# Kernel optimization log

Hardware: AMD Instinct MI355X
Metric: run time of the kernel (lower is better)

The kernel has to match this reference:

```python
import jax, jax.numpy as jnp
import numpy as np

EMBED_DIM = 1024
N_HEADS = 16
HEAD_DIM = EMBED_DIM // N_HEADS
MAX_REL_POS = 2  # hardcoded in the torch module


def _rel_index(length_q, length_k):
    # final_mat[i, j] = clip(i - j, -p, p) + p  with i over k-range, j over q-range
    rq = jnp.arange(length_q)[None, :]
    rk = jnp.arange(length_k)[:, None]
    dist = jnp.clip(rk - rq, -MAX_REL_POS, MAX_REL_POS) + MAX_REL_POS
    return dist  # (len_k, len_q) int; square when len_q == len_k


def setup_inputs() -> dict:
    key = jax.random.key(0)
    ks = jax.random.split(key, 16)
    B, S, E, H, D = 4, 1024, EMBED_DIM, N_HEADS, HEAD_DIM
    xavier = lambda k, shape: jax.random.uniform(
        k, shape, jnp.float32, -1.0, 1.0) * np.sqrt(6.0 / (shape[0] + shape[1]))
    return {
        "query": jax.random.normal(ks[0], (B, S, E), jnp.float32),
        "key": jax.random.normal(ks[1], (B, S, E), jnp.float32),
        "value": jax.random.normal(ks[2], (B, S, E), jnp.float32),
        "Wq": xavier(ks[3], (E, E)), "bq": jnp.zeros((E,), jnp.float32),
        "Wk": xavier(ks[4], (E, E)), "bk": jnp.zeros((E,), jnp.float32),
        "Wv": xavier(ks[5], (E, E)), "bv": jnp.zeros((E,), jnp.float32),
        "Wo": xavier(ks[6], (E, E)), "bo": jnp.zeros((E,), jnp.float32),
        "rpk_table": xavier(ks[7], (2 * MAX_REL_POS + 1, D)),
        "rpv_table": xavier(ks[8], (2 * MAX_REL_POS + 1, D)),
    }


def reference(query, key, value, Wq, bq, Wk, bk, Wv, bv, Wo, bo, rpk_table, rpv_table):
    B, S, E = query.shape
    H, D = N_HEADS, HEAD_DIM
    q = query @ Wq.T + bq
    _k = key @ Wk.T + bk      # computed but unused (faithful to source bug)
    v = value @ Wv.T + bv

    qh = q.reshape(B, S, H, D).transpose(0, 2, 1, 3)   # b h s d
    vh = v.reshape(B, S, H, D).transpose(0, 2, 1, 3)

    # NOTE: source uses query for both sides of the dot product
    dots = jnp.einsum('bhqd,bhkd->bhqk', qh, qh)

    idx = _rel_index(S, S)                              # (S, S)
    rpk = rpk_table[idx]                                # (S, S, D)
    rp_dots = jnp.einsum('bhqd,qkd->bhqk', qh, rpk)

    scale = jnp.sqrt(jnp.asarray(D, q.dtype))
    attn = jax.nn.softmax((dots + rp_dots) / scale, axis=-1)

    weight1 = jnp.einsum('bhqk,bhkd->bhqd', attn, vh)
    rpv = rpv_table[idx]                                # (S, S, D)
    weight2 = jnp.einsum('bhqk,qkd->bhqd', attn, rpv)

    out = (weight1 + weight2).transpose(0, 2, 1, 3).reshape(B, S, E)
    return out @ Wo.T + bo
```

## Files before the change

kernel.cpp:

```cpp
#include <hip/hip_runtime.h>


typedef _Float16 v8h __attribute__((ext_vector_type(8)));
typedef _Float16 v4h __attribute__((ext_vector_type(4)));
typedef float    v4f __attribute__((ext_vector_type(4)));

#define MFMA_F16(A_, B_, C_) __builtin_amdgcn_mfma_f32_16x16x32_f16(A_, B_, C_, 0, 0, 0)

__device__ __forceinline__ void async_copy16(const void* g, void* l) {
    __builtin_amdgcn_global_load_lds(
        (const __attribute__((address_space(1))) void*)g,
        (__attribute__((address_space(3))) void*)l, 16, 0, 0);
}

__device__ __forceinline__ float exp2_hw(float x) {
#if __has_builtin(__builtin_amdgcn_exp2f)
    return __builtin_amdgcn_exp2f(x);
#else
    float r;
    asm("v_exp_f32 %0, %1" : "=v"(r) : "v"(x));
    return r;
#endif
}

__global__ __launch_bounds__(256) void cvt5_kernel(
    const float* __restrict__ s0, const float* __restrict__ s1,
    const float* __restrict__ s2, const float* __restrict__ s3,
    const float* __restrict__ s4,
    _Float16* __restrict__ d0, _Float16* __restrict__ d1,
    _Float16* __restrict__ d2, _Float16* __restrict__ d3,
    _Float16* __restrict__ d4,
    int n0, int n1, int n2, int n3, int n4)
{
    const float* s; _Float16* d; int n;
    switch (blockIdx.y) {
        case 0:  s = s0; d = d0; n = n0; break;
        case 1:  s = s1; d = d1; n = n1; break;
        case 2:  s = s2; d = d2; n = n2; break;
        case 3:  s = s3; d = d3; n = n3; break;
        default: s = s4; d = d4; n = n4; break;
    }
    int i = (blockIdx.x * 256 + threadIdx.x) * 4;
    if (i >= n) return;
    float4 f = *(const float4*)(s + i);
    v4h o = { (_Float16)f.x, (_Float16)f.y, (_Float16)f.z, (_Float16)f.w };
    *(v4h*)(d + i) = o;
}

template<int TM, int MODE>
__device__ __forceinline__ void gemm_core(const _Float16* __restrict__ A,
                                          const _Float16* __restrict__ W,
                                          const float* __restrict__ bias,
                                          void* __restrict__ outp,
                                          int row0, int col0)
{
    constexpr int WCOLS = (TM == 128) ? 64 : 32;
    constexpr int NJ = WCOLS / 16;
    constexpr int SC_H = (MODE == 2) ? 4096 : 64 * WCOLS;
    constexpr int STG_H = (TM + 128) * 64;
    constexpr int TOT_H = (STG_H > 4 * SC_H) ? STG_H : 4 * SC_H;
    __shared__ __align__(16) _Float16 smem[TOT_H];
    _Float16* As = smem;
    _Float16* Bs = smem + TM * 64;

    const int tid  = threadIdx.x;
    const int wave = tid >> 6, lane = tid & 63;
    const int quad = lane >> 4, n16 = lane & 15;
    const int wm = (TM == 128) ? (wave >> 1) : 0;
    const int wn = (TM == 128) ? (wave & 1) : wave;
    const int rL = lane >> 3, c8 = lane & 7;
    const int lcs = c8 ^ rL;

    v4f acc[4][NJ] = {};

    for (int kb = 0; kb < 1024; kb += 64) {
        __syncthreads();
        #pragma unroll
        for (int p = 0; p < TM / 32; p++) {
            int rg = wave * (TM / 32) + p;
            int row = rg * 8 + rL;
            async_copy16(A + (size_t)(row0 + row) * 1024 + kb + lcs * 8, &As[rg * 512]);
        }
        #pragma unroll
        for (int p = 0; p < 4; p++) {
            int rg = wave * 4 + p;
            int row = rg * 8 + rL;
            async_copy16(W + (size_t)(col0 + row) * 1024 + kb + lcs * 8, &Bs[rg * 512]);
        }
        __syncthreads();
        #pragma unroll
        for (int ks = 0; ks < 64; ks += 32) {
            const int pc = ((ks >> 3) + quad) ^ (n16 & 7);
            v8h af[4], bf[NJ];
            #pragma unroll
            for (int i = 0; i < 4; i++)
                af[i] = *(const v8h*)(&As[(wm * 64 + i * 16 + n16) * 64 + pc * 8]);
            #pragma unroll
            for (int j = 0; j < NJ; j++)
                bf[j] = *(const v8h*)(&Bs[(wn * WCOLS + j * 16 + n16) * 64 + pc * 8]);
            #pragma unroll
            for (int i = 0; i < 4; i++)
                #pragma unroll
                for (int j = 0; j < NJ; j++)
                    acc[i][j] = MFMA_F16(af[i], bf[j], acc[i][j]);
        }
    }

    __syncthreads();
    const int b     = (row0 + wm * 64) >> 10;
    const int srow0 = (row0 + wm * 64) & 1023;
    const int C0    = col0 + wn * WCOLS;

    if (MODE == 0) {
        _Float16* sc = smem + wave * SC_H;
        #pragma unroll
        for (int i = 0; i < 4; i++)
            #pragma unroll
            for (int j = 0; j < NJ; j++)
                #pragma unroll
                for (int r = 0; r < 4; r++) {
                    int rowL = i * 16 + quad * 4 + r, colL = j * 16 + n16;
                    float v = acc[i][j][r] + bias[C0 + colL];
                    sc[rowL * 64 + (((colL >> 3) ^ (rowL & 7)) << 3) + (colL & 7)] = (_Float16)v;
                }
        int h = C0 >> 6;
        #pragma unroll
        for (int it = 0; it < 8; it++) {
            int rowR = it * 8 + (lane >> 3), cR = lane & 7;
            v8h val = *(const v8h*)(&sc[rowR * 64 + ((cR ^ (rowR & 7)) << 3)]);
            *(v8h*)((_Float16*)outp +
                    (((size_t)(b * 16 + h) * 1024 + srow0 + rowR) << 6) + cR * 8) = val;
        }
    } else if (MODE == 1) {
        _Float16* sc = smem + wave * SC_H;
        #pragma unroll
        for (int i = 0; i < 4; i++)
            #pragma unroll
            for (int j = 0; j < NJ; j++) {
                int colL = j * 16 + n16;
                int c16 = i * 2 + (quad >> 1);
                v4h pk;
                #pragma unroll
                for (int r = 0; r < 4; r++)
                    pk[r] = (_Float16)(acc[i][j][r] + bias[C0 + colL]);
                *(v4h*)(&sc[colL * 64 + ((c16 ^ (colL & 7)) << 3) + (quad & 1) * 4]) = pk;
            }
        #pragma unroll
        for (int it = 0; it < 8; it++) {
            int dR = it * 8 + (lane >> 3), g = lane & 7;
            v8h val = *(const v8h*)(&sc[dR * 64 + ((g ^ (dR & 7)) << 3)]);
            int cg = C0 + dR;
            int h = cg >> 6, dl = cg & 63;
            _Float16* base = (_Float16*)outp +
                             ((size_t)((b * 16 + h) * 64 + dl) << 10) + srow0;
            int a4  = ((g >> 1) & 1) * 4, b32 = (g >> 2) * 32;
            int p0  = b32 + ((2 * g) & 3) * 8 + a4;
            int p1  = b32 + ((2 * g + 1) & 3) * 8 + a4;
            v4h lo = __builtin_shufflevector(val, val, 0, 1, 2, 3);
            v4h hi = __builtin_shufflevector(val, val, 4, 5, 6, 7);
            *(v4h*)(base + p0) = lo;
            *(v4h*)(base + p1) = hi;
        }
    } else {
        float* sc = (float*)smem + wave * 2048;
        #pragma unroll
        for (int i = 0; i < 4; i++)
            #pragma unroll
            for (int j = 0; j < 2; j++)
                #pragma unroll
                for (int r = 0; r < 4; r++) {
                    int rowL = i * 16 + quad * 4 + r, colL = j * 16 + n16;
                    sc[rowL * 32 + (((colL >> 2) ^ (rowL & 7)) << 2) + (colL & 3)] =
                        acc[i][j][r] + bias[col0 + wn * 32 + colL];
                }
        #pragma unroll
        for (int it = 0; it < 8; it++) {
            int rowR = it * 8 + (lane >> 3), cR = lane & 7;
            v4f val = *(const v4f*)(&sc[rowR * 32 + ((cR ^ (rowR & 7)) << 2)]);
            *(v4f*)((float*)outp + (size_t)(row0 + rowR) * 1024 + col0 + wn * 32 + cR * 4) = val;
        }
    }
}

__global__ __launch_bounds__(256) void gemm_qv_kernel(
    const _Float16* __restrict__ Aq, const _Float16* __restrict__ Av,
    const _Float16* __restrict__ Wq, const _Float16* __restrict__ Wv,
    const float* __restrict__ bq, const float* __restrict__ bv,
    _Float16* __restrict__ q_out, _Float16* __restrict__ v_out)
{
    int id = blockIdx.x;
    int y = (id & 7) | (((id >> 3) & 3) << 3);
    int x = (id >> 5) & 7;
    int z = id >> 8;
    if (z) gemm_core<128, 1>(Av, Wv, bv, (void*)v_out, y * 128, x * 128);
    else   gemm_core<128, 0>(Aq, Wq, bq, (void*)q_out, y * 128, x * 128);
}

__global__ __launch_bounds__(256) void gemm_o_kernel(
    const _Float16* __restrict__ A, const _Float16* __restrict__ W,
    const float* __restrict__ bias, float* __restrict__ outp)
{
    int id = blockIdx.x;
    int y = (id & 7) * 8 + ((id >> 3) & 7);
    int x = id >> 6;
    gemm_core<64, 2>(A, W, bias, (void*)outp, y * 64, x * 128);
}

__global__ __launch_bounds__(256, 4) void attn_kernel(
    const _Float16* __restrict__ qb,
    const _Float16* __restrict__ vt,
    const float* __restrict__ rpk, const float* __restrict__ rpv,
    _Float16* __restrict__ attn_o)
{
    const int blk = blockIdx.x;
    const int bh = blk & 63;
    const int q0 = (blk >> 6) * 64;
    const int tid = threadIdx.x;
    const int wave = tid >> 6, lane = tid & 63;
    const int quad = lane >> 4, n16 = lane & 15;
    const int qw = q0 + wave * 16;
    const _Float16* Qh = qb + (size_t)bh * 1024 * 64;
    const _Float16* Vh = vt + (size_t)bh * 64 * 1024;

    __shared__ __align__(16) _Float16 Ks[2][64 * 64];
    __shared__ __align__(16) _Float16 Vs[2][64 * 64];
    __shared__ float rqs[4][16][5];

    const int rL = lane >> 3, c8 = lane & 7;
    const int lcs = c8 ^ rL;

    #pragma unroll
    for (int p = 0; p < 2; p++) {
        int c = wave * 2 + p;
        int row = c * 8 + rL;
        async_copy16(Qh + (size_t)row * 64 + lcs * 8, &Ks[0][c * 512]);
        async_copy16(Vh + (size_t)row * 1024 + lcs * 8, &Vs[0][c * 512]);
    }

    {
        int m = lane >> 2, seg = lane & 3;
        const _Float16* qrow = Qh + (size_t)(qw + m) * 64 + seg * 16;
        v8h qa = *(const v8h*)(qrow);
        v8h qc = *(const v8h*)(qrow + 8);
        float qd[16];
        #pragma unroll
        for (int x = 0; x < 8; x++) { qd[x] = (float)qa[x]; qd[8 + x] = (float)qc[x]; }
        float qq = 0.f;
        #pragma unroll
        for (int x = 0; x < 16; x++) qq += qd[x] * qd[x];
        qq += __shfl_xor(qq, 1);
        qq += __shfl_xor(qq, 2);
        #pragma unroll
        for (int t = 0; t < 5; t++) {
            float s = 0.f;
            #pragma unroll
            for (int x = 0; x < 16; x++) s += qd[x] * rpk[t * 64 + seg * 16 + x];
            s += __shfl_xor(s, 1);
            s += __shfl_xor(s, 2);
            if (seg == 0) rqs[wave][m][t] = (s - qq) * 0.18033688736f;
        }
    }

    v8h aq0 = *(const v8h*)(Qh + (size_t)(qw + n16) * 64 + quad * 8);
    v8h aq1 = *(const v8h*)(Qh + (size_t)(qw + n16) * 64 + 32 + quad * 8);

    __syncthreads();

    float rc[5];
    #pragma unroll
    for (int t = 0; t < 5; t++) rc[t] = rqs[wave][n16][t];

    float bkt[5] = {0.f, 0.f, 0.f, 0.f, 0.f};
    v4f O[4] = {};

    const int pphys0 = quad ^ (n16 & 7);
    const int pphys1 = (quad + 4) ^ (n16 & 7);
    const float SCL = 0.18033688736f;

    for (int it = 0; it < 16; ++it) {
        const int cur = it & 1;
        const int kb = it * 64;
        if (it + 1 < 16) {
            const int nxt = 1 - cur;
            const int kn = kb + 64;
            #pragma unroll
            for (int p = 0; p < 2; p++) {
                int c = wave * 2 + p;
                int row = c * 8 + rL;
                async_copy16(Qh + (size_t)(kn + row) * 64 + lcs * 8, &Ks[nxt][c * 512]);
                async_copy16(Vh + (size_t)row * 1024 + kn + lcs * 8, &Vs[nxt][c * 512]);
            }
        }

        v8h ak0[4], ak1[4], av0[4], av1[4];
        #pragma unroll
        for (int t = 0; t < 4; t++) {
            ak0[t] = *(const v8h*)(&Ks[cur][(t * 16 + n16) * 64 + pphys0 * 8]);
            ak1[t] = *(const v8h*)(&Ks[cur][(t * 16 + n16) * 64 + pphys1 * 8]);
        }
        #pragma unroll
        for (int dt = 0; dt < 4; dt++) {
            av0[dt] = *(const v8h*)(&Vs[cur][(dt * 16 + n16) * 64 + pphys0 * 8]);
            av1[dt] = *(const v8h*)(&Vs[cur][(dt * 16 + n16) * 64 + pphys1 * 8]);
        }

        int pkLo[4], pkHi[4];
        #pragma unroll
        for (int t = 0; t < 4; t++) {
            v4f s = {0.f, 0.f, 0.f, 0.f};
            s = MFMA_F16(ak0[t], aq0, s);
            s = MFMA_F16(ak1[t], aq1, s);
            const int dqt = qw - kb - t * 16;
            float pv[4];
            if (dqt >= 17) {
                float p0 = exp2_hw(fmaf(s[0], SCL, rc[4]));
                float p1 = exp2_hw(fmaf(s[1], SCL, rc[4]));
                float p2 = exp2_hw(fmaf(s[2], SCL, rc[4]));
                float p3 = exp2_hw(fmaf(s[3], SCL, rc[4]));
                pv[0] = p0; pv[1] = p1; pv[2] = p2; pv[3] = p3;
                bkt[4] += (p0 + p1) + (p2 + p3);
            } else if (dqt <= -17) {
                float p0 = exp2_hw(fmaf(s[0], SCL, rc[0]));
                float p1 = exp2_hw(fmaf(s[1], SCL, rc[0]));
                float p2 = exp2_hw(fmaf(s[2], SCL, rc[0]));
                float p3 = exp2_hw(fmaf(s[3], SCL, rc[0]));
                pv[0] = p0; pv[1] = p1; pv[2] = p2; pv[3] = p3;
                bkt[0] += (p0 + p1) + (p2 + p3);
            } else {
                const int D0 = dqt + n16 - quad * 4;
                #pragma unroll
                for (int r = 0; r < 4; r++) {
                    int diff = D0 - r;
                    float rv = diff >= 2  ? rc[4]
                             : diff == 1  ? rc[3]
                             : diff == 0  ? rc[2]
                             : diff == -1 ? rc[1]
                                          : rc[0];
                    float p = exp2_hw(fmaf(s[r], SCL, rv));
                    pv[r] = p;
                    bkt[4] += (diff >= 2)  ? p : 0.f;
                    bkt[3] += (diff == 1)  ? p : 0.f;
                    bkt[2] += (diff == 0)  ? p : 0.f;
                    bkt[1] += (diff == -1) ? p : 0.f;
                    bkt[0] += (diff <= -2) ? p : 0.f;
                }
            }
            pkLo[t] = __builtin_bit_cast(int, __builtin_amdgcn_cvt_pkrtz(pv[0], pv[1]));
            pkHi[t] = __builtin_bit_cast(int, __builtin_amdgcn_cvt_pkrtz(pv[2], pv[3]));
        }

        union { int d[4]; v8h v; } ub0, ub1;
        ub0.d[0] = pkLo[0]; ub0.d[1] = pkHi[0]; ub0.d[2] = pkLo[1]; ub0.d[3] = pkHi[1];
        ub1.d[0] = pkLo[2]; ub1.d[1] = pkHi[2]; ub1.d[2] = pkLo[3]; ub1.d[3] = pkHi[3];
        v8h bf0 = ub0.v, bf1 = ub1.v;

        #pragma unroll
        for (int dt = 0; dt < 4; dt++) {
            O[dt] = MFMA_F16(av0[dt], bf0, O[dt]);
            O[dt] = MFMA_F16(av1[dt], bf1, O[dt]);
        }

        __syncthreads();
    }

    #pragma unroll
    for (int t = 0; t < 5; t++) {
        bkt[t] += __shfl_xor(bkt[t], 16);
        bkt[t] += __shfl_xor(bkt[t], 32);
    }
    float l = bkt[0] + bkt[1] + bkt[2] + bkt[3] + bkt[4];
    float inv = 1.0f / l;
    int q = qw + n16;
    size_t orow = (size_t)((bh >> 4) * 1024 + q) * 1024 + (bh & 15) * 64;
    #pragma unroll
    for (int dt = 0; dt < 4; dt++) {
        int d0 = dt * 16 + quad * 4;
        v4h st;
        #pragma unroll
        for (int r = 0; r < 4; r++) {
            int d = d0 + r;
            float w2 = bkt[4] * rpv[4 * 64 + d] + bkt[3] * rpv[3 * 64 + d]
                     + bkt[2] * rpv[2 * 64 + d] + bkt[1] * rpv[1 * 64 + d]
                     + bkt[0] * rpv[0 * 64 + d];
            st[r] = (_Float16)((O[dt][r] + w2) * inv);
        }
        *(v4h*)(attn_o + orow + d0) = st;
    }
}

extern "C" void kernel_launch(void* const* d_in, const int* in_sizes, int n_in,
                              void* d_out, int out_size, void* d_ws, size_t ws_size,
                              hipStream_t stream)
{
    const float* query = (const float*)d_in[0];
    const float* value = (const float*)d_in[2];
    const float* Wq = (const float*)d_in[3];
    const float* bq = (const float*)d_in[4];
    const float* Wv = (const float*)d_in[7];
    const float* bv = (const float*)d_in[8];
    const float* Wo = (const float*)d_in[9];
    const float* bo = (const float*)d_in[10];
    const float* rpk = (const float*)d_in[11];
    const float* rpv = (const float*)d_in[12];
    float* out = (float*)d_out;

    char* ws = (char*)d_ws;
    const size_t MB = 1024 * 1024;
    _Float16* q_bhsd = (_Float16*)(ws);
    _Float16* v_t    = (_Float16*)(ws + 8 * MB);
    _Float16* q16    = (_Float16*)(ws + 16 * MB);
    _Float16* attn_o = (_Float16*)(ws + 16 * MB);
    _Float16* v16    = (_Float16*)(ws + 24 * MB);
    _Float16* wq16   = (_Float16*)(ws + 32 * MB);
    _Float16* wv16   = (_Float16*)(ws + 34 * MB);
    _Float16* wo16   = (_Float16*)(ws + 36 * MB);

    cvt5_kernel<<<dim3(4096, 5), 256, 0, stream>>>(
        query, value, Wq, Wv, Wo, q16, v16, wq16, wv16, wo16,
        4096 * 1024, 4096 * 1024, 1024 * 1024, 1024 * 1024, 1024 * 1024);

    gemm_qv_kernel<<<dim3(512), 256, 0, stream>>>(
        q16, v16, wq16, wv16, bq, bv, q_bhsd, v_t);

    attn_kernel<<<dim3(1024), 256, 0, stream>>>(q_bhsd, v_t, rpk, rpv, attn_o);

    gemm_o_kernel<<<dim3(512), 256, 0, stream>>>(attn_o, wo16, bo, out);
}
```

Baseline: 196.0 us.

## Software-pipeline QK scores one tile ahead and single-buffer V in LDS

Restructures the attention loop so the QK^T MFMA scores for the next key tile are computed while the current tile's exponentials and PV products are processed. K tiles are prefetched two iterations ahead, and V is reduced to a single LDS buffer loaded at the start of each iteration. A second barrier is added mid-iteration before V is read. The aim is to overlap MFMA latency with the softmax VALU work and cut LDS use. In exchange, V loads are no longer prefetched across iterations, there are more barriers, and register pressure rises from holding two score sets.

```diff
diff --git a/kernel.cpp b/kernel.cpp
--- a/kernel.cpp
+++ b/kernel.cpp
@@ -223,7 +223,7 @@
     const _Float16* Vh = vt + (size_t)bh * 64 * 1024;
 
     __shared__ __align__(16) _Float16 Ks[2][64 * 64];
-    __shared__ __align__(16) _Float16 Vs[2][64 * 64];
+    __shared__ __align__(16) _Float16 Vs[64 * 64];
     __shared__ float rqs[4][16][5];
 
     const int rL = lane >> 3, c8 = lane & 7;
@@ -234,7 +234,7 @@
         int c = wave * 2 + p;
         int row = c * 8 + rL;
         async_copy16(Qh + (size_t)row * 64 + lcs * 8, &Ks[0][c * 512]);
-        async_copy16(Vh + (size_t)row * 1024 + lcs * 8, &Vs[0][c * 512]);
+        async_copy16(Qh + (size_t)(64 + row) * 64 + lcs * 8, &Ks[1][c * 512]);
     }
 
     {
@@ -270,46 +270,59 @@
     #pragma unroll
     for (int t = 0; t < 5; t++) rc[t] = rqs[wave][n16][t];
 
-    float bkt[5] = {0.f, 0.f, 0.f, 0.f, 0.f};
-    v4f O[4] = {};
-
     const int pphys0 = quad ^ (n16 & 7);
     const int pphys1 = (quad + 4) ^ (n16 & 7);
     const float SCL = 0.18033688736f;
 
+    v4f scur[4];
+    #pragma unroll
+    for (int t = 0; t < 4; t++) {
+        v8h k0 = *(const v8h*)(&Ks[0][(t * 16 + n16) * 64 + pphys0 * 8]);
+        v8h k1 = *(const v8h*)(&Ks[0][(t * 16 + n16) * 64 + pphys1 * 8]);
+        v4f s = {0.f, 0.f, 0.f, 0.f};
+        s = MFMA_F16(k0, aq0, s);
+        scur[t] = MFMA_F16(k1, aq1, s);
+    }
+    __syncthreads();
+
+    float bkt[5] = {0.f, 0.f, 0.f, 0.f, 0.f};
+    v4f O[4] = {};
+
     for (int it = 0; it < 16; ++it) {
-        const int cur = it & 1;
         const int kb = it * 64;
-        if (it + 1 < 16) {
-            const int nxt = 1 - cur;
-            const int kn = kb + 64;
+
+        #pragma unroll
+        for (int p = 0; p < 2; p++) {
+            int c = wave * 2 + p;
+            int row = c * 8 + rL;
+            async_copy16(Vh + (size_t)row * 1024 + kb + lcs * 8, &Vs[c * 512]);
+        }
+        if (it + 2 < 16) {
+            const int kn = kb + 128;
             #pragma unroll
             for (int p = 0; p < 2; p++) {
                 int c = wave * 2 + p;
                 int row = c * 8 + rL;
-                async_copy16(Qh + (size_t)(kn + row) * 64 + lcs * 8, &Ks[nxt][c * 512]);
-                async_copy16(Vh + (size_t)row * 1024 + kn + lcs * 8, &Vs[nxt][c * 512]);
+                async_copy16(Qh + (size_t)(kn + row) * 64 + lcs * 8, &Ks[it & 1][c * 512]);
             }
         }
 
-        v8h ak0[4], ak1[4], av0[4], av1[4];
+        v4f snx[4] = {};
+        if (it + 1 < 16) {
+            #pragma unroll
+            for (int t = 0; t < 4; t++) {
+                v8h k0 = *(const v8h*)(&Ks[(it + 1) & 1][(t * 16 + n16) * 64 + pphys0 * 8]);
+                v8h k1 = *(const v8h*)(&Ks[(it + 1) & 1][(t * 16 + n16) * 64 + pphys1 * 8]);
+                v4f s = {0.f, 0.f, 0.f, 0.f};
+                s = MFMA_F16(k0, aq0, s);
+                snx[t] = MFMA_F16(k1, aq1, s);
+            }
+        }
+
+        int pkLo[4], pkHi[4];
         #pragma unroll
         for (int t = 0; t < 4; t++) {
-            ak0[t] = *(const v8h*)(&Ks[cur][(t * 16 + n16) * 64 + pphys0 * 8]);
-            ak1[t] = *(const v8h*)(&Ks[cur][(t * 16 + n16) * 64 + pphys1 * 8]);
-        }
-        #pragma unroll
-        for (int dt = 0; dt < 4; dt++) {
-            av0[dt] = *(const v8h*)(&Vs[cur][(dt * 16 + n16) * 64 + pphys0 * 8]);
-            av1[dt] = *(const v8h*)(&Vs[cur][(dt * 16 + n16) * 64 + pphys1 * 8]);
-        }
-
-        int pkLo[4], pkHi[4];
-        #pragma unroll
-        for (int t = 0; t < 4; t++) {
-            v4f s = {0.f, 0.f, 0.f, 0.f};
-            s = MFMA_F16(ak0[t], aq0, s);
-            s = MFMA_F16(ak1[t], aq1, s);
+            const v4f s = scur[t];
             const int dqt = qw - kb - t * 16;
             float pv[4];
             if (dqt >= 17) {
@@ -349,6 +362,8 @@
             pkHi[t] = __builtin_bit_cast(int, __builtin_amdgcn_cvt_pkrtz(pv[2], pv[3]));
         }
 
+        __syncthreads();
+
         union { int d[4]; v8h v; } ub0, ub1;
         ub0.d[0] = pkLo[0]; ub0.d[1] = pkHi[0]; ub0.d[2] = pkLo[1]; ub0.d[3] = pkHi[1];
         ub1.d[0] = pkLo[2]; ub1.d[1] = pkHi[2]; ub1.d[2] = pkLo[3]; ub1.d[3] = pkHi[3];
@@ -356,11 +371,17 @@
 
         #pragma unroll
         for (int dt = 0; dt < 4; dt++) {
-            O[dt] = MFMA_F16(av0[dt], bf0, O[dt]);
-            O[dt] = MFMA_F16(av1[dt], bf1, O[dt]);
+            const int rowd = (dt * 16 + n16) * 64;
+            v8h av0 = *(const v8h*)(&Vs[rowd + pphys0 * 8]);
+            v8h av1 = *(const v8h*)(&Vs[rowd + pphys1 * 8]);
+            O[dt] = MFMA_F16(av0, bf0, O[dt]);
+            O[dt] = MFMA_F16(av1, bf1, O[dt]);
         }
 
         __syncthreads();
+
+        #pragma unroll
+        for (int t = 0; t < 4; t++) scur[t] = snx[t];
     }
 
     #pragma unroll
```

After: 193.1 us, median of 2. About the same (-1.5%).
